# Optimization experiments

Measured on AMD Instinct MI355X. Metric: run time of the kernel, lower is better.

Reference implementation:

```python
import jax, jax.numpy as jnp
import numpy as np

B, C, T = 4, 1024, 2048
H = 16            # num_heads
G = 32            # GroupNorm groups (normalization(channels) == GroupNorm(32, C))
EPS = 1e-5


def setup_inputs() -> dict:
    key = jax.random.key(0)
    ks = jax.random.split(key, 7)
    x = jax.random.normal(ks[0], (B, C, T), dtype=jnp.float32)
    gn_scale = jax.random.normal(ks[1], (C,), dtype=jnp.float32) * 0.02 + 1.0
    gn_bias = jax.random.normal(ks[2], (C,), dtype=jnp.float32) * 0.02
    qkv_w = jax.random.normal(ks[3], (3 * C, C), dtype=jnp.float32) / np.sqrt(C)
    qkv_b = jax.random.normal(ks[4], (3 * C,), dtype=jnp.float32) * 0.02
    # NOTE: original zero-inits proj_out; randomized here so output != x for testing.
    proj_w = jax.random.normal(ks[5], (C, C), dtype=jnp.float32) / np.sqrt(C)
    proj_b = jax.random.normal(ks[6], (C,), dtype=jnp.float32) * 0.02
    return {"x": x, "gn_scale": gn_scale, "gn_bias": gn_bias,
            "qkv_w": qkv_w, "qkv_b": qkv_b, "proj_w": proj_w, "proj_b": proj_b}


def reference(x, gn_scale, gn_bias, qkv_w, qkv_b, proj_w, proj_b):
    b, c, t = x.shape
    ch = c // H
    # GroupNorm(32, C) over (channels-in-group, T)
    xg = x.reshape(b, G, c // G, t)
    mean = xg.mean(axis=(2, 3), keepdims=True)
    var = xg.var(axis=(2, 3), keepdims=True)
    xn = ((xg - mean) * jax.lax.rsqrt(var + EPS)).reshape(b, c, t)
    xn = xn * gn_scale[None, :, None] + gn_bias[None, :, None]
    # 1x1 conv QKV: [B, 3C, T]
    qkv = jnp.einsum('oc,bct->bot', qkv_w, xn) + qkv_b[None, :, None]
    q, k, v = jnp.split(qkv, 3, axis=1)
    # split heads -> [B*H, ch, T]
    q = q.reshape(b * H, ch, t)
    k = k.reshape(b * H, ch, t)
    v = v.reshape(b * H, ch, t)
    scale = 1.0 / np.sqrt(np.sqrt(ch)).astype(np.float32)
    # full T x T attention weights, softmax in fp32 (as original)
    w = jnp.einsum('bct,bcs->bts', q * scale, k * scale)
    w = jax.nn.softmax(w.astype(jnp.float32), axis=-1).astype(w.dtype)
    a = jnp.einsum('bts,bcs->bct', w, v).reshape(b, c, t)
    # 1x1 conv projection + residual
    h = jnp.einsum('oc,bct->bot', proj_w, a) + proj_b[None, :, None]
    return x + h
```

## Files before the change

kernel.cpp:

```cpp
#include <hip/hip_runtime.h>
#include <hip/hip_bf16.h>
#include <stdint.h>

#define Bn 4
#define Cn 1024
#define Tn 2048
#define Hn 16
#define Gn 32
#define SCALE_Q 0.18033688f

typedef short short8  __attribute__((ext_vector_type(8)));
typedef short short4_t __attribute__((ext_vector_type(4)));
typedef float float4_t __attribute__((ext_vector_type(4)));
typedef unsigned int uint2_t __attribute__((ext_vector_type(2)));

__device__ __forceinline__ short f2bf(float f) {
    uint32_t u = __float_as_uint(f);
    uint32_t r = (u + 0x7FFFu + ((u >> 16) & 1u)) >> 16;
    return (short)r;
}

__device__ __forceinline__ float exp2_fast(float x) {
#if __has_builtin(__builtin_amdgcn_exp2f)
    return __builtin_amdgcn_exp2f(x);
#else
    return exp2f(x);
#endif
}

__device__ __forceinline__ uint32_t pack_bf16_trunc(float lo, float hi) {
#if __has_builtin(__builtin_amdgcn_perm)
    return __builtin_amdgcn_perm(__float_as_uint(hi), __float_as_uint(lo), 0x07060302u);
#else
    return (__float_as_uint(lo) >> 16) | (__float_as_uint(hi) & 0xFFFF0000u);
#endif
}

__device__ __forceinline__ void permswap32(uint32_t& x, uint32_t& y) {
#if __has_builtin(__builtin_amdgcn_permlane32_swap)
    uint2_t r = __builtin_amdgcn_permlane32_swap(x, y, false, false);
    x = r[0]; y = r[1];
#else
    asm volatile("v_permlane32_swap_b32 %0, %1" : "+v"(x), "+v"(y));
#endif
}
__device__ __forceinline__ void permswap16(uint32_t& x, uint32_t& y) {
#if __has_builtin(__builtin_amdgcn_permlane16_swap)
    uint2_t r = __builtin_amdgcn_permlane16_swap(x, y, false, false);
    x = r[0]; y = r[1];
#else
    asm volatile("v_permlane16_swap_b32 %0, %1" : "+v"(x), "+v"(y));
#endif
}

#define GLL16(gptr, lptr)                                                      \
    __builtin_amdgcn_global_load_lds(                                          \
        (const __attribute__((address_space(1))) unsigned int*)(gptr),         \
        (__attribute__((address_space(3))) unsigned int*)(lptr), 16, 0, 0)

__global__ __launch_bounds__(256) void cvt_w(const float* __restrict__ src,
                                             short* __restrict__ dst, int n4) {
    int i = blockIdx.x * 256 + threadIdx.x;
    if (i < n4) {
        float4_t v = reinterpret_cast<const float4_t*>(src)[i];
        short4_t o;
        o[0] = f2bf(v[0]); o[1] = f2bf(v[1]); o[2] = f2bf(v[2]); o[3] = f2bf(v[3]);
        reinterpret_cast<short4_t*>(dst)[i] = o;
    }
}

__global__ __launch_bounds__(256) void groupnorm_k(const float* __restrict__ x,
                                                   const float* __restrict__ gs,
                                                   const float* __restrict__ gb,
                                                   short* __restrict__ xnT) {
    int blk = blockIdx.x;
    int b = blk >> 5, g = blk & 31;
    const float* base = x + ((size_t)(b * Cn + g * 32)) * Tn;
    int tid = threadIdx.x;

    float s = 0.f, ss = 0.f;
    const float4_t* b4 = reinterpret_cast<const float4_t*>(base);
    for (int i = tid; i < 16384; i += 256) {
        float4_t v = b4[i];
        s  += v[0] + v[1] + v[2] + v[3];
        ss += v[0]*v[0] + v[1]*v[1] + v[2]*v[2] + v[3]*v[3];
    }
    #pragma unroll
    for (int m = 1; m < 64; m <<= 1) { s += __shfl_xor(s, m); ss += __shfl_xor(ss, m); }
    __shared__ float red[8];
    int wave = tid >> 6;
    if ((tid & 63) == 0) { red[wave * 2] = s; red[wave * 2 + 1] = ss; }
    __syncthreads();
    float ts  = red[0] + red[2] + red[4] + red[6];
    float tss = red[1] + red[3] + red[5] + red[7];
    float mean = ts * (1.f / 65536.f);
    float var  = tss * (1.f / 65536.f) - mean * mean;
    float rstd = rsqrtf(var + 1e-5f);

    __shared__ float tile[64][33];
    for (int t0 = 0; t0 < Tn; t0 += 64) {
        #pragma unroll
        for (int k = 0; k < 8; k++) {
            int e = tid + k * 256;
            int c = e >> 6, tt = e & 63;
            float v = base[c * Tn + t0 + tt];
            tile[tt][c] = (v - mean) * rstd * gs[g * 32 + c] + gb[g * 32 + c];
        }
        __syncthreads();
        #pragma unroll
        for (int k = 0; k < 8; k++) {
            int f = tid + k * 256;
            int tt = f >> 5, c = f & 31;
            xnT[((size_t)(b * Tn + t0 + tt)) * Cn + g * 32 + c] = f2bf(tile[tt][c]);
        }
        __syncthreads();
    }
}

template <int MODE>
__global__ __launch_bounds__(256) void gemm_k(const short* __restrict__ W,
                                              const short* __restrict__ Bm,
                                              const float* __restrict__ bias,
                                              const float* __restrict__ xres,
                                              short* __restrict__ qkT,
                                              short* __restrict__ vbuf,
                                              float* __restrict__ outp) {
    constexpr int K = 1024;
    constexpr int NT = K / 64;
    __shared__ short As[2][128 * 64];
    __shared__ short Bs[2][128 * 64];

    int Nx = gridDim.x, Ny = gridDim.y;
    int lin = blockIdx.x + Nx * (blockIdx.y + Ny * blockIdx.z);
    int chunk = (Nx * Ny * (int)gridDim.z) >> 3;
    int nl = (lin & 7) * chunk + (lin >> 3);
    int bx = nl % Nx; int rest = nl / Nx;
    int by = rest % Ny; int bz = rest / Ny;

    int m0 = bx * 128, n0 = by * 128, b = bz;
    int tid = threadIdx.x;
    int wave = tid >> 6, lane = tid & 63, quad = lane >> 4, l15 = lane & 15;
    int wm = wave >> 1, wn = wave & 1;
    const short* Ab = W + (size_t)m0 * K;
    const short* Bb = Bm + ((size_t)b * Tn + n0) * K;

    float4_t acc[4][4];
    float4_t z = {0.f, 0.f, 0.f, 0.f};
    #pragma unroll
    for (int i = 0; i < 4; i++)
        #pragma unroll
        for (int j = 0; j < 4; j++) acc[i][j] = z;

    int sw = l15 & 7;

    auto stage = [&](int buf, int k0) {
        #pragma unroll
        for (int r = 0; r < 4; r++) {
            int cid = r * 256 + tid;
            int row = cid >> 3, j = cid & 7;
            int ch = j ^ (row & 7);
            GLL16(Ab + (size_t)row * K + k0 + ch * 8, &As[buf][cid * 8]);
            GLL16(Bb + (size_t)row * K + k0 + ch * 8, &Bs[buf][cid * 8]);
        }
    };

    stage(0, 0);
    __syncthreads();

    for (int it = 0; it < NT; ++it) {
        int cur = it & 1;
        if (it + 1 < NT) stage(cur ^ 1, (it + 1) * 64);
        #pragma unroll
        for (int kk = 0; kk < 2; kk++) {
            short8 af[4], bfg[4];
            #pragma unroll
            for (int mi = 0; mi < 4; mi++)
                af[mi] = *reinterpret_cast<const short8*>(
                    &As[cur][(wm * 64 + mi * 16 + l15) * 64 + ((4 * kk + quad) ^ sw) * 8]);
            #pragma unroll
            for (int ni = 0; ni < 4; ni++)
                bfg[ni] = *reinterpret_cast<const short8*>(
                    &Bs[cur][(wn * 64 + ni * 16 + l15) * 64 + ((4 * kk + quad) ^ sw) * 8]);
            #pragma unroll
            for (int mi = 0; mi < 4; mi++)
                #pragma unroll
                for (int ni = 0; ni < 4; ni++)
                    acc[mi][ni] = __builtin_amdgcn_mfma_f32_16x16x32_bf16(
                        af[mi], bfg[ni], acc[mi][ni], 0, 0, 0);
        }
        __syncthreads();
    }

    if (MODE == 0) {
        #pragma unroll
        for (int mi = 0; mi < 4; mi++) {
            int mrow = m0 + wm * 64 + mi * 16 + quad * 4;
            #pragma unroll
            for (int ni = 0; ni < 4; ni++) {
                int t = n0 + wn * 64 + ni * 16 + l15;
                if (mrow < 2048) {
                    int hh = mrow >> 6, ch = mrow & 63;
                    float sc = (mrow < 1024) ? SCALE_Q : 1.0f;
                    short4_t pk;
                    #pragma unroll
                    for (int r = 0; r < 4; r++)
                        pk[r] = f2bf((acc[mi][ni][r] + bias[mrow + r]) * sc);
                    *reinterpret_cast<short4_t*>(
                        &qkT[(((size_t)b * 32 + hh) * Tn + t) * 64 + ch]) = pk;
                } else {
                    int c = mrow - 2048;
                    #pragma unroll
                    for (int r = 0; r < 4; r++)
                        vbuf[((size_t)b * Cn + c + r) * Tn + t] =
                            f2bf(acc[mi][ni][r] + bias[mrow + r]);
                }
            }
        }
    } else {
        #pragma unroll
        for (int mi = 0; mi < 4; mi++) {
            int mrow = m0 + wm * 64 + mi * 16 + quad * 4;
            #pragma unroll
            for (int ni = 0; ni < 4; ni++) {
                int t = n0 + wn * 64 + ni * 16 + l15;
                #pragma unroll
                for (int r = 0; r < 4; r++) {
                    size_t idx = ((size_t)b * Cn + mrow + r) * Tn + t;
                    outp[idx] = xres[idx] + bias[mrow + r] + acc[mi][ni][r];
                }
            }
        }
    }
}

__global__ __launch_bounds__(512, 4) void attn_k(const short* __restrict__ qkT,
                                                 const short* __restrict__ vbuf,
                                                 short* __restrict__ aT) {
    __shared__ short ks[2][64 * 72];
    __shared__ short vs[2][64 * 72];
    int bh = blockIdx.y; int b = bh >> 4, h = bh & 15;
    int t0 = blockIdx.x * 256;
    int tid = threadIdx.x;
    int wave = tid >> 6, lane = tid & 63, quad = lane >> 4, l15 = lane & 15;
    const short* qb = qkT + (((size_t)b * 32 + h) * Tn) * 64;
    const short* kb = qkT + (((size_t)b * 32 + 16 + h) * Tn) * 64;
    const short* vb = vbuf + ((size_t)b * Cn + h * 64) * Tn;
    int tw = t0 + wave * 32;

    short8 qf[2][2];
    #pragma unroll
    for (int tni = 0; tni < 2; tni++)
        #pragma unroll
        for (int kk = 0; kk < 2; kk++)
            qf[tni][kk] = *reinterpret_cast<const short8*>(
                qb + ((size_t)(tw + tni * 16 + l15)) * 64 + kk * 32 + quad * 8);

    short8 ones;
    #pragma unroll
    for (int i = 0; i < 8; i++) ones[i] = (short)0x3F80;

    float4_t z = {0.f, 0.f, 0.f, 0.f};
    float4_t acc[2][4], lacc[2];
    #pragma unroll
    for (int i = 0; i < 2; i++) {
        lacc[i] = z;
        #pragma unroll
        for (int j = 0; j < 4; j++) acc[i][j] = z;
    }

    int srow = tid >> 3, soff = (tid & 7) * 8;
    const short* kgp = kb + (size_t)srow * 64 + soff;
    const short* vgp = vb + (size_t)srow * Tn + soff;
    short* krd = &ks[0][0]; short* kwr = &ks[1][0];
    short* vrd = &vs[0][0]; short* vwr = &vs[1][0];
    int sdst = srow * 72 + soff;

    {
        uint4 k0v = *reinterpret_cast<const uint4*>(kgp);
        uint4 v0v = *reinterpret_cast<const uint4*>(vgp);
        *reinterpret_cast<uint4*>(&krd[sdst]) = k0v;
        *reinterpret_cast<uint4*>(&vrd[sdst]) = v0v;
    }
    __syncthreads();

    for (int it = 0; it < Tn / 64; ++it) {
        uint4 knx, vnx;
        if (it < Tn / 64 - 1) {
            knx = *reinterpret_cast<const uint4*>(kgp + (size_t)(it + 1) * 64 * 64);
            vnx = *reinterpret_cast<const uint4*>(vgp + (size_t)(it + 1) * 64);
        }

        #pragma unroll
        for (int pr = 0; pr < 2; pr++) {
            uint32_t pk[2][2][2];
            #pragma unroll
            for (int half = 0; half < 2; half++) {
                int smi = pr * 2 + half;
                float4_t sa[2] = {z, z};
                __builtin_amdgcn_s_setprio(1);
                #pragma unroll
                for (int kk = 0; kk < 2; kk++) {
                    short8 kf = *reinterpret_cast<const short8*>(
                        &krd[(smi * 16 + l15) * 72 + kk * 32 + quad * 8]);
                    #pragma unroll
                    for (int tni = 0; tni < 2; tni++)
                        sa[tni] = __builtin_amdgcn_mfma_f32_16x16x32_bf16(
                            kf, qf[tni][kk], sa[tni], 0, 0, 0);
                }
                __builtin_amdgcn_s_setprio(0);
                #pragma unroll
                for (int tni = 0; tni < 2; tni++) {
                    float p0 = exp2_fast(sa[tni][0]);
                    float p1 = exp2_fast(sa[tni][1]);
                    float p2 = exp2_fast(sa[tni][2]);
                    float p3 = exp2_fast(sa[tni][3]);
                    pk[half][tni][0] = pack_bf16_trunc(p0, p1);
                    pk[half][tni][1] = pack_bf16_trunc(p2, p3);
                }
            }
            short8 vf[4];
            #pragma unroll
            for (int ci = 0; ci < 4; ci++)
                vf[ci] = *reinterpret_cast<const short8*>(
                    &vrd[(ci * 16 + l15) * 72 + pr * 32 + quad * 8]);
            #pragma unroll
            for (int tni = 0; tni < 2; tni++) {
                uint32_t x0 = pk[0][tni][0], y0 = pk[1][tni][0];
                permswap32(x0, y0); permswap16(x0, y0);
                uint32_t x1 = pk[0][tni][1], y1 = pk[1][tni][1];
                permswap32(x1, y1); permswap16(x1, y1);
                uint4 afu = {x0, x1, y0, y1};
                short8 af = *reinterpret_cast<short8*>(&afu);
                __builtin_amdgcn_s_setprio(1);
                lacc[tni] = __builtin_amdgcn_mfma_f32_16x16x32_bf16(
                    af, ones, lacc[tni], 0, 0, 0);
                #pragma unroll
                for (int ci = 0; ci < 4; ci++)
                    acc[tni][ci] = __builtin_amdgcn_mfma_f32_16x16x32_bf16(
                        af, vf[ci], acc[tni][ci], 0, 0, 0);
                __builtin_amdgcn_s_setprio(0);
            }
        }

        if (it < Tn / 64 - 1) {
            *reinterpret_cast<uint4*>(&kwr[sdst]) = knx;
            *reinterpret_cast<uint4*>(&vwr[sdst]) = vnx;
        }
        __syncthreads();
        short* tk = krd; krd = kwr; kwr = tk;
        short* tv = vrd; vrd = vwr; vwr = tv;
    }

    #pragma unroll
    for (int tni = 0; tni < 2; tni++) {
        #pragma unroll
        for (int r = 0; r < 4; r++) {
            float rl = 1.0f / lacc[tni][r];
            int t = tw + tni * 16 + quad * 4 + r;
            #pragma unroll
            for (int ci = 0; ci < 4; ci++) {
                int ch = ci * 16 + l15;
                aT[((size_t)b * Tn + t) * Cn + h * 64 + ch] =
                    f2bf(acc[tni][ci][r] * rl);
            }
        }
    }
}

extern "C" void kernel_launch(void* const* d_in, const int* in_sizes, int n_in,
                              void* d_out, int out_size, void* d_ws, size_t ws_size,
                              hipStream_t stream) {
    const float* x     = (const float*)d_in[0];
    const float* gs    = (const float*)d_in[1];
    const float* gb    = (const float*)d_in[2];
    const float* qkvw  = (const float*)d_in[3];
    const float* qkvb  = (const float*)d_in[4];
    const float* projw = (const float*)d_in[5];
    const float* projb = (const float*)d_in[6];
    float* out = (float*)d_out;

    char* ws = (char*)d_ws;
    short* wqkv  = (short*)(ws + 0);
    short* wproj = (short*)(ws + 6291456);
    short* xnT   = (short*)(ws + 8388608);
    short* aT    = (short*)(ws + 8388608);
    short* qkT   = (short*)(ws + 25165824);
    short* vbuf  = (short*)(ws + 58720256);

    cvt_w<<<dim3(3072), dim3(256), 0, stream>>>(qkvw, wqkv, 786432);
    cvt_w<<<dim3(1024), dim3(256), 0, stream>>>(projw, wproj, 262144);
    groupnorm_k<<<dim3(Bn * Gn), dim3(256), 0, stream>>>(x, gs, gb, xnT);
    gemm_k<0><<<dim3(24, 16, 4), dim3(256), 0, stream>>>(wqkv, xnT, qkvb, nullptr,
                                                         qkT, vbuf, nullptr);
    attn_k<<<dim3(8, 64), dim3(512), 0, stream>>>(qkT, vbuf, aT);
    gemm_k<1><<<dim3(8, 16, 4), dim3(256), 0, stream>>>(wproj, aT, projb, x,
                                                        nullptr, nullptr, out);
}
```

Before: 328.1 us.

## Deepen GEMM global-to-LDS prefetch to two tiles ahead with explicit vmcnt waits

Reworks the GEMM main loop so the direct global-to-LDS loads run two K-tiles ahead instead of one. It uses explicit s_waitcnt vmcnt counts and raw s_barrier with sched_barrier fences in place of the full __syncthreads drain. It also drops the XCD-aware block index remapping and uses plain blockIdx. The aim is to hide global load latency behind MFMA work, at the cost of hand-tuned wait counts that depend on the exact number of loads issued per stage and a possible loss of L2 locality across XCDs.

```diff
diff --git a/kernel.cpp b/kernel.cpp
--- a/kernel.cpp
+++ b/kernel.cpp
@@ -130,14 +130,7 @@
     __shared__ short As[2][128 * 64];
     __shared__ short Bs[2][128 * 64];
 
-    int Nx = gridDim.x, Ny = gridDim.y;
-    int lin = blockIdx.x + Nx * (blockIdx.y + Ny * blockIdx.z);
-    int chunk = (Nx * Ny * (int)gridDim.z) >> 3;
-    int nl = (lin & 7) * chunk + (lin >> 3);
-    int bx = nl % Nx; int rest = nl / Nx;
-    int by = rest % Ny; int bz = rest / Ny;
-
-    int m0 = bx * 128, n0 = by * 128, b = bz;
+    int m0 = blockIdx.x * 128, n0 = blockIdx.y * 128, b = blockIdx.z;
     int tid = threadIdx.x;
     int wave = tid >> 6, lane = tid & 63, quad = lane >> 4, l15 = lane & 15;
     int wm = wave >> 1, wn = wave & 1;
@@ -165,11 +158,15 @@
     };
 
     stage(0, 0);
-    __syncthreads();
+    stage(1, 64);
+    __builtin_amdgcn_sched_barrier(0);
+    asm volatile("s_waitcnt vmcnt(8)" ::: "memory");
+    __builtin_amdgcn_sched_barrier(0);
+    __builtin_amdgcn_s_barrier();
+    __builtin_amdgcn_sched_barrier(0);
 
     for (int it = 0; it < NT; ++it) {
         int cur = it & 1;
-        if (it + 1 < NT) stage(cur ^ 1, (it + 1) * 64);
         #pragma unroll
         for (int kk = 0; kk < 2; kk++) {
             short8 af[4], bfg[4];
@@ -188,7 +185,19 @@
                     acc[mi][ni] = __builtin_amdgcn_mfma_f32_16x16x32_bf16(
                         af[mi], bfg[ni], acc[mi][ni], 0, 0, 0);
         }
-        __syncthreads();
+        __builtin_amdgcn_sched_barrier(0);
+        __builtin_amdgcn_s_barrier();
+        __builtin_amdgcn_sched_barrier(0);
+        if (it + 2 < NT) stage(cur, (it + 2) * 64);
+        __builtin_amdgcn_sched_barrier(0);
+        if (it + 2 < NT) {
+            asm volatile("s_waitcnt vmcnt(8)" ::: "memory");
+        } else if (it + 1 < NT) {
+            asm volatile("s_waitcnt vmcnt(0)" ::: "memory");
+        }
+        __builtin_amdgcn_sched_barrier(0);
+        __builtin_amdgcn_s_barrier();
+        __builtin_amdgcn_sched_barrier(0);
     }
 
     if (MODE == 0) {
```

Result: faster. 311.2 us (-5.2%).
